# Kernel tuning notes

Hardware: AMD Instinct MI355X
Metric: run time of the kernel (lower is better)

## Reference

```python
import jax, jax.numpy as jnp
import numpy as np

DIM = 768
NUM_HEADS = 12
HEAD_DIM = DIM // NUM_HEADS
ALL_HEAD_DIM = HEAD_DIM * NUM_HEADS
SCALE = HEAD_DIM ** -0.5


def setup_inputs() -> dict:
    key = jax.random.key(0)
    k1, k2, k3, k4 = jax.random.split(key, 4)
    B, N = 8, 1024
    x = jax.random.normal(k1, (B, N, DIM), dtype=jnp.float32)
    # qkv_bias=False -> no qkv bias; proj has bias (nn.Linear default)
    w_qkv = jax.random.normal(k2, (DIM, 3 * ALL_HEAD_DIM), dtype=jnp.float32) * (DIM ** -0.5)
    w_proj = jax.random.normal(k3, (ALL_HEAD_DIM, DIM), dtype=jnp.float32) * (ALL_HEAD_DIM ** -0.5)
    b_proj = jax.random.normal(k4, (DIM,), dtype=jnp.float32) * 0.02
    return {"x": x, "w_qkv": w_qkv, "w_proj": w_proj, "b_proj": b_proj}


def reference(x, w_qkv, w_proj, b_proj):
    B, N, C = x.shape
    qkv = (x @ w_qkv).reshape(B, N, 3, NUM_HEADS, HEAD_DIM)
    qkv = jnp.transpose(qkv, (2, 0, 3, 1, 4))  # [3, B, H, N, D]
    q, k, v = qkv[0], qkv[1], qkv[2]
    attn = jax.nn.softmax(jnp.einsum('bhnd,bhmd->bhnm', q * SCALE, k), axis=-1)
    out = jnp.einsum('bhnm,bhmd->bhnd', attn, v)  # [B, H, N, D]
    out = jnp.transpose(out, (0, 2, 1, 3)).reshape(B, N, ALL_HEAD_DIM)
    return out @ w_proj + b_proj
```

## Files before the change

### kernel.cpp

```cpp
#include <hip/hip_runtime.h>

#define NH 12
#define HD 64
#define SEQ 1024
#define BATCH 8
#define DIM 768
#define QKVN 2304
#define ROWS 8192

typedef __bf16 bf16x8 __attribute__((ext_vector_type(8)));
typedef float f32x4 __attribute__((ext_vector_type(4)));
typedef unsigned short u16x8 __attribute__((ext_vector_type(8)));
typedef unsigned short u16x4 __attribute__((ext_vector_type(4)));
typedef short s16x4 __attribute__((ext_vector_type(4)));

__device__ __forceinline__ unsigned short f2bf(float f) {
  union { float f; unsigned int u; } c; c.f = f;
  unsigned int u = c.u;
  u += 0x7fffu + ((u >> 16) & 1u);
  return (unsigned short)(u >> 16);
}

__device__ __forceinline__ void gload_lds16(const unsigned short* g, unsigned short* l) {
  __builtin_amdgcn_global_load_lds(
      (const __attribute__((address_space(1))) void*)g,
      (__attribute__((address_space(3))) void*)l, 16, 0, 0);
}

__device__ __forceinline__ void tr_tile(const float* __restrict__ src, unsigned short* __restrict__ dst,
                                        int R, int C, int bx, int by, float tile[32][33]) {
  int tx = threadIdx.x & 31, ty = threadIdx.x >> 5;
  int c0 = bx * 32, r0 = by * 32;
#pragma unroll
  for (int i = 0; i < 4; ++i)
    tile[ty + i * 8][tx] = src[(size_t)(r0 + ty + i * 8) * C + c0 + tx];
  __syncthreads();
#pragma unroll
  for (int i = 0; i < 4; ++i)
    dst[(size_t)(c0 + ty + i * 8) * R + r0 + tx] = f2bf(tile[tx][ty + i * 8]);
}

__global__ void prep_kernel(const float* __restrict__ x, unsigned short* __restrict__ xb,
                            const float* __restrict__ w_qkv, unsigned short* __restrict__ wqkvT,
                            const float* __restrict__ w_proj, unsigned short* __restrict__ wprojT) {
  __shared__ float tile[32][33];
  int blk = blockIdx.x;
  if (blk < 6144) {
    int i = blk * 256 + threadIdx.x;
    float4 v = ((const float4*)x)[i];
    u16x4 o;
    o.x = f2bf(v.x); o.y = f2bf(v.y); o.z = f2bf(v.z); o.w = f2bf(v.w);
    ((u16x4*)xb)[i] = o;
  } else if (blk < 6144 + 1728) {
    int t = blk - 6144;
    tr_tile(w_qkv, wqkvT, DIM, QKVN, t % 72, t / 72, tile);
  } else {
    int t = blk - 6144 - 1728;
    tr_tile(w_proj, wprojT, DIM, DIM, t % 24, t / 24, tile);
  }
}

template <bool BF16_OUT, bool SCALE_Q>
__global__ __launch_bounds__(256, 5) void gemm64(
    const unsigned short* __restrict__ A, const unsigned short* __restrict__ BT,
    void* __restrict__ Cout, const float* __restrict__ bias,
    int M, int N, int K, int nbyXCD) {
  __shared__ unsigned short As[2][128 * 32];
  __shared__ unsigned short Bs[2][64 * 32];
  const int tid = threadIdx.x;
  const int wave = tid >> 6, lane = tid & 63, quad = lane >> 4, l16 = lane & 15;
  const int g = blockIdx.x & 7, bi = blockIdx.x >> 3;
  const int by = g * nbyXCD + (bi % nbyXCD);
  const int bx = bi / nbyXCD;
  const int bm = by * 128, bn = bx * 64;

  const int r0 = tid >> 2, kc0 = (tid & 3) * 8;
  const unsigned short* Ag = A + (size_t)(bm + r0) * K + kc0;
  const unsigned short* Bg = BT + (size_t)(bn + r0) * K + kc0;
  unsigned short* AsB = &As[0][0];
  unsigned short* BsB = &Bs[0][0];
  const int wdst = (tid & ~63) * 8;

#define STAGE_G(kt, b) do {                                                    \
    int koff_ = (kt) * 32;                                                     \
    gload_lds16(Ag + koff_,                  AsB + (b) * 4096 + wdst);         \
    gload_lds16(Ag + koff_ + (size_t)64 * K, AsB + (b) * 4096 + wdst + 2048);  \
    gload_lds16(Bg + koff_,                  BsB + (b) * 2048 + wdst);         \
  } while (0)

  f32x4 zero4 = {0.f, 0.f, 0.f, 0.f};
  f32x4 acc[2][4];
#pragma unroll
  for (int i = 0; i < 2; ++i)
#pragma unroll
    for (int j = 0; j < 4; ++j) acc[i][j] = zero4;

  const int nkt = K >> 5;
  STAGE_G(0, 0);
  for (int kt = 0; kt < nkt; ++kt) {
    __syncthreads();
    if (kt + 1 < nkt) STAGE_G(kt + 1, (kt + 1) & 1);
    const unsigned short* Ab = AsB + (kt & 1) * 4096;
    const unsigned short* Bb = BsB + (kt & 1) * 2048;
    bf16x8 af[2], bf[4];
#pragma unroll
    for (int mt = 0; mt < 2; ++mt)
      af[mt] = *(const bf16x8*)&Ab[(wave * 32 + mt * 16 + l16) * 32 + quad * 8];
#pragma unroll
    for (int nt = 0; nt < 4; ++nt)
      bf[nt] = *(const bf16x8*)&Bb[(nt * 16 + l16) * 32 + quad * 8];
#pragma unroll
    for (int mt = 0; mt < 2; ++mt)
#pragma unroll
      for (int nt = 0; nt < 4; ++nt)
        acc[mt][nt] = __builtin_amdgcn_mfma_f32_16x16x32_bf16(af[mt], bf[nt], acc[mt][nt], 0, 0, 0);
  }
#undef STAGE_G

#pragma unroll
  for (int mt = 0; mt < 2; ++mt)
#pragma unroll
    for (int nt = 0; nt < 4; ++nt) {
      int col = bn + nt * 16 + l16;
      float bv = BF16_OUT ? 0.f : bias[col];
      float scl = (SCALE_Q && col < DIM) ? 0.125f : 1.0f;
#pragma unroll
      for (int r = 0; r < 4; ++r) {
        int row = bm + wave * 32 + mt * 16 + quad * 4 + r;
        float v = acc[mt][nt][r];
        if (BF16_OUT)
          ((unsigned short*)Cout)[(size_t)row * N + col] = f2bf(v * scl);
        else
          ((float*)Cout)[(size_t)row * N + col] = v + bv;
      }
    }
}

#define VS 76
__global__ __launch_bounds__(512, 6) void attn_kernel(
    const unsigned short* __restrict__ qkv, unsigned short* __restrict__ out) {
  __shared__ unsigned short Ks[2][64 * 64];
  __shared__ unsigned short Vts[2][64 * VS];

  const int tid = threadIdx.x;
  const int wave = tid >> 6, lane = tid & 63, quad = lane >> 4, l16 = lane & 15;
  const int x = blockIdx.x;
  const int qt = (x >> 3) & 7;
  const int bh = (x & 7) + 8 * (x >> 6);
  const int b = bh / NH, h = bh % NH;
  const int qcol = h * HD, kcol = DIM + h * HD, vcol = 2 * DIM + h * HD;
  const int rowQ0 = b * SEQ + qt * 128;
  const int rowKV0 = b * SEQ;

  const int kk_s = tid >> 8, rem_s = tid & 255, n_s = rem_s >> 2, kc_s = rem_s & 3;
  const unsigned short* kgp = qkv + (size_t)(rowKV0 + n_s) * QKVN + kcol + kk_s * 32 + kc_s * 8;
  unsigned short* klp = &Ks[0][0] + (tid & ~63) * 8;
  const int vn = tid & 63, vd0 = (tid >> 6) * 8;
  const unsigned short* vgp = qkv + (size_t)(rowKV0 + vn) * QKVN + vcol + vd0;

  bf16x8 qf[2];
  {
    const unsigned short* qp = qkv + (size_t)(rowQ0 + wave * 16 + l16) * QKVN + qcol + quad * 8;
    qf[0] = *(const bf16x8*)qp;
    qf[1] = *(const bf16x8*)(qp + 32);
  }

  u16x8 vreg = *(const u16x8*)vgp;
  gload_lds16(kgp, klp);
  {
    unsigned short* vb = &Vts[0][0];
#pragma unroll
    for (int e = 0; e < 8; ++e)
      vb[(vd0 + e) * VS + vn] = vreg[e];
  }

  f32x4 zero4 = {0.f, 0.f, 0.f, 0.f};
  f32x4 o[4];
#pragma unroll
  for (int dt = 0; dt < 4; ++dt) o[dt] = zero4;
  float lsum = 0.f;

  for (int jt = 0; jt < 16; ++jt) {
    u16x8 vnext;
    if (jt < 15) vnext = *(const u16x8*)(vgp + (size_t)(jt + 1) * 64 * QKVN);
    __syncthreads();
    if (jt < 15)
      gload_lds16(kgp + (size_t)(jt + 1) * 64 * QKVN, klp + ((jt + 1) & 1) * 4096);

    const unsigned short* Kb = &Ks[jt & 1][0];
    const unsigned short* Vb = &Vts[jt & 1][0];

    f32x4 s[4];
#pragma unroll
    for (int nt = 0; nt < 4; ++nt) s[nt] = zero4;
#pragma unroll
    for (int kk = 0; kk < 2; ++kk)
#pragma unroll
      for (int nt = 0; nt < 4; ++nt) {
        bf16x8 kf = *(const bf16x8*)&Kb[kk * 2048 + (nt * 16 + l16) * 32 + quad * 8];
        s[nt] = __builtin_amdgcn_mfma_f32_16x16x32_bf16(kf, qf[kk], s[nt], 0, 0, 0);
      }

    s16x4 pf[4];
#pragma unroll
    for (int nt = 0; nt < 4; ++nt)
#pragma unroll
      for (int r = 0; r < 4; ++r) {
        float p = __expf(s[nt][r]);
        lsum += p;
        pf[nt][r] = (short)f2bf(p);
      }

#pragma unroll
    for (int nt = 0; nt < 4; ++nt)
#pragma unroll
      for (int dt = 0; dt < 4; ++dt) {
        s16x4 vv = *(const s16x4*)&Vb[(dt * 16 + l16) * VS + nt * 16 + quad * 4];
        o[dt] = __builtin_amdgcn_mfma_f32_16x16x16bf16_1k(pf[nt], vv, o[dt], 0, 0, 0);
      }

    if (jt < 15) {
      unsigned short* vb = &Vts[(jt + 1) & 1][0];
#pragma unroll
      for (int e = 0; e < 8; ++e)
        vb[(vd0 + e) * VS + vn] = vnext[e];
    }
  }

  float l = lsum;
  l += __shfl_xor(l, 16);
  l += __shfl_xor(l, 32);
#pragma unroll
  for (int r = 0; r < 4; ++r) {
    float inv = 1.f / __shfl(l, quad * 4 + r);
    int row = rowQ0 + wave * 16 + quad * 4 + r;
#pragma unroll
    for (int dt = 0; dt < 4; ++dt)
      out[(size_t)row * DIM + h * HD + dt * 16 + l16] = f2bf(o[dt][r] * inv);
  }
}

extern "C" void kernel_launch(void* const* d_in, const int* in_sizes, int n_in,
                              void* d_out, int out_size, void* d_ws, size_t ws_size,
                              hipStream_t stream) {
  const float* x = (const float*)d_in[0];
  const float* w_qkv = (const float*)d_in[1];
  const float* w_proj = (const float*)d_in[2];
  const float* b_proj = (const float*)d_in[3];
  float* outp = (float*)d_out;

  unsigned short* xb = (unsigned short*)d_ws;
  unsigned short* wqkvT = xb + (size_t)ROWS * DIM;
  unsigned short* wprojT = wqkvT + (size_t)QKVN * DIM;
  unsigned short* qkvb = wprojT + (size_t)DIM * DIM;
  unsigned short* attnb = xb;

  prep_kernel<<<dim3(6144 + 1728 + 576), 256, 0, stream>>>(x, xb, w_qkv, wqkvT, w_proj, wprojT);
  gemm64<true, true><<<dim3(2304), 256, 0, stream>>>(xb, wqkvT, qkvb, nullptr, ROWS, QKVN, DIM, 8);
  attn_kernel<<<dim3(8 * 96), 512, 0, stream>>>(qkvb, attnb);
  gemm64<false, false><<<dim3(768), 256, 0, stream>>>(attnb, wprojT, outp, b_proj, ROWS, DIM, DIM, 8);
}
```

Measured before the change: 192.2 us.

## Replace LDS-staged GEMM with register-direct global loads and 128x128 tiles

Both projection GEMMs drop the double-buffered LDS staging and instead have each wave load its MFMA operand fragments directly from global memory into registers. The K loop is fully unrolled with K as a template parameter. The block tile grows from 128x64 to 128x128, with four waves each computing 64x64. This removes LDS traffic and barriers, but every wave now re-reads operands from global memory or cache with no on-chip sharing inside the block, uses more registers (occupancy bound lowered to 3), and issues strided 16-byte loads that may coalesce poorly.

After: 281.7 us. +46.6%, slower.

```diff
diff --git a/kernel.cpp b/kernel.cpp
--- a/kernel.cpp
+++ b/kernel.cpp
@@ -60,73 +60,55 @@
   }
 }
 
-template <bool BF16_OUT, bool SCALE_Q>
-__global__ __launch_bounds__(256, 5) void gemm64(
+template <bool BF16_OUT, bool SCALE_Q, int K>
+__global__ __launch_bounds__(256, 3) void gemm_reg(
     const unsigned short* __restrict__ A, const unsigned short* __restrict__ BT,
     void* __restrict__ Cout, const float* __restrict__ bias,
-    int M, int N, int K, int nbyXCD) {
-  __shared__ unsigned short As[2][128 * 32];
-  __shared__ unsigned short Bs[2][64 * 32];
+    int M, int N, int nbyXCD) {
   const int tid = threadIdx.x;
   const int wave = tid >> 6, lane = tid & 63, quad = lane >> 4, l16 = lane & 15;
+  const int wm = wave >> 1, wn = wave & 1;
   const int g = blockIdx.x & 7, bi = blockIdx.x >> 3;
   const int by = g * nbyXCD + (bi % nbyXCD);
   const int bx = bi / nbyXCD;
-  const int bm = by * 128, bn = bx * 64;
-
-  const int r0 = tid >> 2, kc0 = (tid & 3) * 8;
-  const unsigned short* Ag = A + (size_t)(bm + r0) * K + kc0;
-  const unsigned short* Bg = BT + (size_t)(bn + r0) * K + kc0;
-  unsigned short* AsB = &As[0][0];
-  unsigned short* BsB = &Bs[0][0];
-  const int wdst = (tid & ~63) * 8;
-
-#define STAGE_G(kt, b) do {                                                    \
-    int koff_ = (kt) * 32;                                                     \
-    gload_lds16(Ag + koff_,                  AsB + (b) * 4096 + wdst);         \
-    gload_lds16(Ag + koff_ + (size_t)64 * K, AsB + (b) * 4096 + wdst + 2048);  \
-    gload_lds16(Bg + koff_,                  BsB + (b) * 2048 + wdst);         \
-  } while (0)
+  const int bm = by * 128, bn = bx * 128;
+
+  const unsigned short* Ap = A + (size_t)(bm + wm * 64 + l16) * K + quad * 8;
+  const unsigned short* Bp = BT + (size_t)(bn + wn * 64 + l16) * K + quad * 8;
 
   f32x4 zero4 = {0.f, 0.f, 0.f, 0.f};
-  f32x4 acc[2][4];
-#pragma unroll
-  for (int i = 0; i < 2; ++i)
+  f32x4 acc[4][4];
+#pragma unroll
+  for (int i = 0; i < 4; ++i)
 #pragma unroll
     for (int j = 0; j < 4; ++j) acc[i][j] = zero4;
 
-  const int nkt = K >> 5;
-  STAGE_G(0, 0);
-  for (int kt = 0; kt < nkt; ++kt) {
-    __syncthreads();
-    if (kt + 1 < nkt) STAGE_G(kt + 1, (kt + 1) & 1);
-    const unsigned short* Ab = AsB + (kt & 1) * 4096;
-    const unsigned short* Bb = BsB + (kt & 1) * 2048;
-    bf16x8 af[2], bf[4];
-#pragma unroll
-    for (int mt = 0; mt < 2; ++mt)
-      af[mt] = *(const bf16x8*)&Ab[(wave * 32 + mt * 16 + l16) * 32 + quad * 8];
+#pragma unroll
+  for (int kt = 0; kt < K / 32; ++kt) {
+    bf16x8 af[4], bf[4];
+#pragma unroll
+    for (int mt = 0; mt < 4; ++mt)
+      af[mt] = *(const bf16x8*)(Ap + (size_t)mt * 16 * K + kt * 32);
 #pragma unroll
     for (int nt = 0; nt < 4; ++nt)
-      bf[nt] = *(const bf16x8*)&Bb[(nt * 16 + l16) * 32 + quad * 8];
-#pragma unroll
-    for (int mt = 0; mt < 2; ++mt)
+      bf[nt] = *(const bf16x8*)(Bp + (size_t)nt * 16 * K + kt * 32);
+#pragma unroll
+    for (int mt = 0; mt < 4; ++mt)
 #pragma unroll
       for (int nt = 0; nt < 4; ++nt)
         acc[mt][nt] = __builtin_amdgcn_mfma_f32_16x16x32_bf16(af[mt], bf[nt], acc[mt][nt], 0, 0, 0);
   }
-#undef STAGE_G
-
-#pragma unroll
-  for (int mt = 0; mt < 2; ++mt)
+
+#pragma unroll
+  for (int mt = 0; mt < 4; ++mt)
 #pragma unroll
     for (int nt = 0; nt < 4; ++nt) {
-      int col = bn + nt * 16 + l16;
+      int col = bn + wn * 64 + nt * 16 + l16;
       float bv = BF16_OUT ? 0.f : bias[col];
       float scl = (SCALE_Q && col < DIM) ? 0.125f : 1.0f;
 #pragma unroll
       for (int r = 0; r < 4; ++r) {
-        int row = bm + wave * 32 + mt * 16 + quad * 4 + r;
+        int row = bm + wm * 64 + mt * 16 + quad * 4 + r;
         float v = acc[mt][nt][r];
         if (BF16_OUT)
           ((unsigned short*)Cout)[(size_t)row * N + col] = f2bf(v * scl);
@@ -256,7 +238,7 @@
   unsigned short* attnb = xb;
 
   prep_kernel<<<dim3(6144 + 1728 + 576), 256, 0, stream>>>(x, xb, w_qkv, wqkvT, w_proj, wprojT);
-  gemm64<true, true><<<dim3(2304), 256, 0, stream>>>(xb, wqkvT, qkvb, nullptr, ROWS, QKVN, DIM, 8);
+  gemm_reg<true, true, DIM><<<dim3(1152), 256, 0, stream>>>(xb, wqkvT, qkvb, nullptr, ROWS, QKVN, 8);
   attn_kernel<<<dim3(8 * 96), 512, 0, stream>>>(qkvb, attnb);
-  gemm64<false, false><<<dim3(768), 256, 0, stream>>>(attnb, wprojT, outp, b_proj, ROWS, DIM, DIM, 8);
-}
+  gemm_reg<false, false, DIM><<<dim3(384), 256, 0, stream>>>(attnb, wprojT, outp, b_proj, ROWS, DIM, 8);
+}
```
